# Optimization experiments

Measured on AMD Instinct MI355X. Metric: run time of the kernel, lower is better.

Reference implementation:

```python
import jax, jax.numpy as jnp
import numpy as np

B, N, C = 4, 2048, 1024
HEADS, DHEAD = 16, 64
EPS = 1e-7
SCALE = DHEAD ** (-0.5)


def setup_inputs() -> dict:
    key = jax.random.key(0)
    k1, k2, k3, k4 = jax.random.split(key, 4)
    inner = HEADS * DHEAD
    return {
        "x": jax.random.normal(k1, (B, N, C), dtype=jnp.float32),
        "gamma": jnp.ones((1, 1, C), dtype=jnp.float32),
        "Wq": jax.random.normal(k2, (inner, C), dtype=jnp.float32) * np.sqrt(1.0 / C),
        "Wkv": jax.random.normal(k3, (2 * DHEAD, C), dtype=jnp.float32) * np.sqrt(1.0 / C),
        "Wo": jax.random.normal(k4, (C, inner), dtype=jnp.float32) * np.sqrt(1.0 / inner) * 1e-5,
        "ls_scale": jnp.full((C,), 1e-4, dtype=jnp.float32),
    }


def reference(x, gamma, Wq, Wkv, Wo, ls_scale):
    # BiasFreeLayerNorm: divide by unbiased std (no mean subtraction), scale by gamma
    std = jnp.std(x, axis=-1, ddof=1, keepdims=True)
    xn = (x / (std + EPS)) * gamma
    # q from normalized x, k/v from the ORIGINAL x (kv_input = x before norm)
    q = xn @ Wq.T                       # [B, N, H*D]
    kv = x @ Wkv.T                      # [B, N, 2*D]
    k, v = kv[..., :DHEAD], kv[..., DHEAD:]  # shared single kv head (MQA)
    q = q.reshape(B, N, HEADS, DHEAD).transpose(0, 2, 1, 3) * SCALE  # [B, H, N, D]
    sim = jnp.einsum('bhid,bjd->bhij', q, k)
    attn = jax.nn.softmax(sim, axis=-1)
    out = jnp.einsum('bhij,bjd->bhid', attn, v)       # [B, H, N, D]
    out = out.transpose(0, 2, 1, 3).reshape(B, N, HEADS * DHEAD)
    out = out @ Wo.T
    return ls_scale * out
```

## Files before the change

kernel.cpp:

```cpp
#include <hip/hip_runtime.h>
#include <hip/hip_bf16.h>
#include <stdint.h>

typedef __attribute__((ext_vector_type(8))) short short8;
typedef __attribute__((ext_vector_type(4))) short short4v;
typedef __attribute__((ext_vector_type(4))) float f32x4;
typedef __attribute__((ext_vector_type(4))) unsigned short us4;

#define B_ 4
#define N_ 2048
#define C_ 1024
#define H_ 16
#define D_ 64

__device__ __forceinline__ unsigned short f2bf(float f) {
  union { float f; unsigned u; } v; v.f = f;
  unsigned u = v.u;
  u += 0x7fffu + ((u >> 16) & 1u);
  return (unsigned short)(u >> 16);
}

__device__ __forceinline__ unsigned short bfc(float f) {
  union { __hip_bfloat16 h; unsigned short u; } v;
  v.h = __float2bfloat16(f);
  return v.u;
}

__device__ __forceinline__ void glds16(const unsigned short* g, const unsigned short* l) {
  __builtin_amdgcn_global_load_lds(
      (const __attribute__((address_space(1))) void*)(uintptr_t)g,
      (__attribute__((address_space(3))) void*)(uintptr_t)l, 16, 0, 0);
}

__device__ __forceinline__ f32x4 mfma16(short8 a, short8 b, f32x4 c) {
  return __builtin_amdgcn_mfma_f32_16x16x32_bf16(a, b, c, 0, 0, 0);
}

#if __has_builtin(__builtin_amdgcn_mfma_f32_16x16x16bf16_1k)
__device__ __forceinline__ f32x4 mfma16b(short4v a, short4v b, f32x4 c) {
  return __builtin_amdgcn_mfma_f32_16x16x16bf16_1k(a, b, c, 0, 0, 0);
}
#else
__device__ __forceinline__ f32x4 mfma16b(short4v a, short4v b, f32x4 c) {
  asm volatile("v_mfma_f32_16x16x16_bf16 %0, %1, %2, %0\n\ts_nop 7\n\ts_nop 7"
               : "+v"(c) : "v"(a), "v"(b));
  return c;
}
#endif

__global__ __launch_bounds__(256) void prep_cast_k(const float* __restrict__ x,
                                                   const float* __restrict__ gamma,
                                                   unsigned short* __restrict__ xb,
                                                   float* __restrict__ rstd_v,
                                                   const float* __restrict__ wq,
                                                   const float* __restrict__ wkv,
                                                   const float* __restrict__ wo,
                                                   unsigned short* __restrict__ dq,
                                                   unsigned short* __restrict__ dkv,
                                                   unsigned short* __restrict__ dwo) {
  const int t = threadIdx.x;
  if (blockIdx.x >= 8192) {
    const int i = (blockIdx.x - 8192) * 256 + t;
    if (i < 262144) {
      const float4 v = ((const float4*)wq)[i];
      const float4 gv = ((const float4*)gamma)[i & 255];
      us4 o;
      o.x = f2bf(v.x * gv.x); o.y = f2bf(v.y * gv.y);
      o.z = f2bf(v.z * gv.z); o.w = f2bf(v.w * gv.w);
      ((us4*)dq)[i] = o;
    } else {
      const float* s;
      unsigned short* d;
      int j;
      if (i < 294912) { s = wkv; d = dkv; j = i - 262144; }
      else { s = wo; d = dwo; j = i - 294912; }
      const float4 v = ((const float4*)s)[j];
      us4 o; o.x = f2bf(v.x); o.y = f2bf(v.y); o.z = f2bf(v.z); o.w = f2bf(v.w);
      ((us4*)d)[j] = o;
    }
    return;
  }
  const int row = blockIdx.x;
  const float4 v = ((const float4*)(x + (size_t)row * C_))[t];
  float s1 = v.x + v.y + v.z + v.w;
  float s2 = v.x * v.x + v.y * v.y + v.z * v.z + v.w * v.w;
#pragma unroll
  for (int off = 32; off > 0; off >>= 1) {
    s1 += __shfl_down(s1, off);
    s2 += __shfl_down(s2, off);
  }
  __shared__ float r1[4], r2[4];
  if ((t & 63) == 0) { r1[t >> 6] = s1; r2[t >> 6] = s2; }
  __syncthreads();
  s1 = r1[0] + r1[1] + r1[2] + r1[3];
  s2 = r2[0] + r2[1] + r2[2] + r2[3];
  const float var = (s2 - s1 * s1 * (1.0f / C_)) * (1.0f / (C_ - 1));
  const float rstd = 1.0f / (sqrtf(var) + 1e-7f);
  if (t == 0) rstd_v[row] = rstd;
  us4 a;
  a.x = f2bf(v.x); a.y = f2bf(v.y); a.z = f2bf(v.z); a.w = f2bf(v.w);
  ((us4*)(xb + (size_t)row * C_))[t] = a;
}

__global__ __launch_bounds__(256, 2) void qkv_gemm(const unsigned short* __restrict__ xb,
                                                   const unsigned short* __restrict__ wq,
                                                   const unsigned short* __restrict__ wkv,
                                                   const float* __restrict__ rstd_v,
                                                   unsigned short* __restrict__ qo,
                                                   unsigned short* __restrict__ kvo,
                                                   unsigned short* __restrict__ vtb) {
  const bool iskv = (blockIdx.x == 8);
  const unsigned short* Bw = iskv ? wkv : wq;
  const int n0 = iskv ? 0 : blockIdx.x * 128;
  const int K = 1024, m0 = blockIdx.y * 128;

  __shared__ unsigned short At[128 * 32];
  __shared__ unsigned short Bt[128 * 32];
  const int t = threadIdx.x;
  const int w = t >> 6, l = t & 63;
  const int ql = l & 15, g = l >> 4;
  const int wr = (w >> 1) * 64, wc = (w & 1) * 64;

  const int pr0 = t >> 2, pb0 = t & 3;
  const int lb0 = pb0 ^ ((pr0 >> 1) & 3);
  const int pr1 = 64 + (t >> 2);
  const int lb1 = pb0 ^ ((pr1 >> 1) & 3);
  const unsigned short* Ab = xb + (size_t)m0 * K;
  const unsigned short* Bb = Bw + (size_t)n0 * K;

  f32x4 acc[4][4];
#pragma unroll
  for (int i = 0; i < 4; ++i)
#pragma unroll
    for (int j = 0; j < 4; ++j) acc[i][j] = f32x4{0.f, 0.f, 0.f, 0.f};

  for (int k0 = 0; k0 < K; k0 += 32) {
    glds16(Ab + (size_t)pr0 * K + k0 + lb0 * 8, &At[w * 512]);
    glds16(Ab + (size_t)pr1 * K + k0 + lb1 * 8, &At[2048 + w * 512]);
    glds16(Bb + (size_t)pr0 * K + k0 + lb0 * 8, &Bt[w * 512]);
    glds16(Bb + (size_t)pr1 * K + k0 + lb1 * 8, &Bt[2048 + w * 512]);
    __syncthreads();
    short8 af[4], bfr[4];
#pragma unroll
    for (int i = 0; i < 4; ++i) {
      const int row = wr + i * 16 + ql;
      af[i] = *(const short8*)&At[row * 32 + ((g ^ ((row >> 1) & 3)) * 8)];
    }
#pragma unroll
    for (int i = 0; i < 4; ++i) {
      const int row = wc + i * 16 + ql;
      bfr[i] = *(const short8*)&Bt[row * 32 + ((g ^ ((row >> 1) & 3)) * 8)];
    }
#pragma unroll
    for (int mi = 0; mi < 4; ++mi)
#pragma unroll
      for (int ni = 0; ni < 4; ++ni)
        acc[mi][ni] = mfma16(af[mi], bfr[ni], acc[mi][ni]);
    __syncthreads();
  }

  if (!iskv) {
    float rs[4][4];
#pragma unroll
    for (int mi = 0; mi < 4; ++mi)
#pragma unroll
      for (int r = 0; r < 4; ++r)
        rs[mi][r] = 0.18033688011112042f * rstd_v[m0 + wr + mi * 16 + g * 4 + r];
#pragma unroll
    for (int mi = 0; mi < 4; ++mi)
#pragma unroll
      for (int ni = 0; ni < 4; ++ni) {
        const int col = n0 + wc + ni * 16 + ql;
#pragma unroll
        for (int r = 0; r < 4; ++r) {
          const int row = m0 + wr + mi * 16 + g * 4 + r;
          qo[(size_t)row * 1024 + col] = f2bf(acc[mi][ni][r] * rs[mi][r]);
        }
      }
  } else if (wc == 0) {
#pragma unroll
    for (int mi = 0; mi < 4; ++mi)
#pragma unroll
      for (int ni = 0; ni < 4; ++ni) {
        const int col = ni * 16 + ql;
#pragma unroll
        for (int r = 0; r < 4; ++r) {
          const int row = m0 + wr + mi * 16 + g * 4 + r;
          kvo[(size_t)row * 128 + col] = f2bf(acc[mi][ni][r]);
        }
      }
  } else {
    const int brow = m0 >> 11;
    unsigned short* vb = vtb + (size_t)brow * 64 * 2048;
#pragma unroll
    for (int mi = 0; mi < 4; ++mi) {
      const int nbase = (m0 & 2047) + wr + mi * 16 + g * 4;
#pragma unroll
      for (int ni = 0; ni < 4; ++ni) {
        const int d = ni * 16 + ql;
        const int nadj = nbase ^ (((d >> 3) & 1) ? 4 : 0);
        us4 st;
        st.x = f2bf(acc[mi][ni][0]);
        st.y = f2bf(acc[mi][ni][1]);
        st.z = f2bf(acc[mi][ni][2]);
        st.w = f2bf(acc[mi][ni][3]);
        *(us4*)&vb[(size_t)d * 2048 + nadj] = st;
      }
    }
  }
}

__global__ __launch_bounds__(256, 2) void gemm_o(const unsigned short* __restrict__ A,
                                                 const unsigned short* __restrict__ Bw,
                                                 float* __restrict__ Cout,
                                                 const float* __restrict__ colscale,
                                                 int M, int N, int K) {
  __shared__ unsigned short At[128 * 32];
  __shared__ unsigned short Bt[128 * 32];
  const int t = threadIdx.x;
  const int w = t >> 6, l = t & 63;
  const int ql = l & 15, g = l >> 4;
  const int wr = (w >> 1) * 64, wc = (w & 1) * 64;
  const int m0 = blockIdx.y * 128, n0 = blockIdx.x * 128;

  const int pr0 = t >> 2, pb0 = t & 3;
  const int lb0 = pb0 ^ ((pr0 >> 1) & 3);
  const int pr1 = 64 + (t >> 2);
  const int lb1 = pb0 ^ ((pr1 >> 1) & 3);
  const unsigned short* Ab = A + (size_t)m0 * K;
  const unsigned short* Bb = Bw + (size_t)n0 * K;

  f32x4 acc[4][4];
#pragma unroll
  for (int i = 0; i < 4; ++i)
#pragma unroll
    for (int j = 0; j < 4; ++j) acc[i][j] = f32x4{0.f, 0.f, 0.f, 0.f};

  for (int k0 = 0; k0 < K; k0 += 32) {
    glds16(Ab + (size_t)pr0 * K + k0 + lb0 * 8, &At[w * 512]);
    glds16(Ab + (size_t)pr1 * K + k0 + lb1 * 8, &At[2048 + w * 512]);
    glds16(Bb + (size_t)pr0 * K + k0 + lb0 * 8, &Bt[w * 512]);
    glds16(Bb + (size_t)pr1 * K + k0 + lb1 * 8, &Bt[2048 + w * 512]);
    __syncthreads();
    short8 af[4], bfr[4];
#pragma unroll
    for (int i = 0; i < 4; ++i) {
      const int row = wr + i * 16 + ql;
      af[i] = *(const short8*)&At[row * 32 + ((g ^ ((row >> 1) & 3)) * 8)];
    }
#pragma unroll
    for (int i = 0; i < 4; ++i) {
      const int row = wc + i * 16 + ql;
      bfr[i] = *(const short8*)&Bt[row * 32 + ((g ^ ((row >> 1) & 3)) * 8)];
    }
#pragma unroll
    for (int mi = 0; mi < 4; ++mi)
#pragma unroll
      for (int ni = 0; ni < 4; ++ni)
        acc[mi][ni] = mfma16(af[mi], bfr[ni], acc[mi][ni]);
    __syncthreads();
  }

#pragma unroll
  for (int mi = 0; mi < 4; ++mi)
#pragma unroll
    for (int ni = 0; ni < 4; ++ni) {
      const int col = n0 + wc + ni * 16 + ql;
      const float cs = colscale[col];
#pragma unroll
      for (int r = 0; r < 4; ++r) {
        const int row = m0 + wr + mi * 16 + g * 4 + r;
        Cout[(size_t)row * N + col] = acc[mi][ni][r] * cs;
      }
    }
}

__global__ __launch_bounds__(256, 3) void attn_k(const unsigned short* __restrict__ qb,
                                                 const unsigned short* __restrict__ kvb,
                                                 const unsigned short* __restrict__ vtb,
                                                 unsigned short* __restrict__ ao) {
  __shared__ unsigned short Kt[2][64 * 64];
  __shared__ unsigned short Vt[2][64 * 64];

  const int idx = blockIdx.x;
  const int qc = idx & 15, hd = (idx >> 4) & 15, b = idx >> 8;
  const int t = threadIdx.x, w = t >> 6, l = t & 63;
  const int ql = l & 15, g = l >> 4;
  const int q0 = qc * 128 + w * 32;

  const unsigned short* qbase = qb + (size_t)(b * N_ + q0) * C_ + hd * D_;
  short8 Qf[2][2];
#pragma unroll
  for (int qs = 0; qs < 2; ++qs)
#pragma unroll
    for (int h = 0; h < 2; ++h)
      Qf[qs][h] = *(const short8*)(qbase + (size_t)(16 * qs + ql) * C_ + 32 * h + 8 * g);

  const unsigned short* kvrow = kvb + (size_t)(b * N_) * 128;
  const unsigned short* vtrow = vtb + (size_t)b * 64 * 2048;
  const int sr = l >> 3;
  const int blk = ((l & 7) ^ sr) << 3;
  const int row0 = 16 * w + sr;
  const int row1 = row0 + 8;
  const int sw = ql & 7;
  const int hb = (ql >> 3) & 1;

  auto stage = [&](int bi, int kt) {
    glds16(kvrow + (size_t)(kt * 64 + row0) * 128 + blk, &Kt[bi][(2 * w) * 512]);
    glds16(kvrow + (size_t)(kt * 64 + row1) * 128 + blk, &Kt[bi][(2 * w + 1) * 512]);
    glds16(vtrow + (size_t)row0 * 2048 + kt * 64 + blk, &Vt[bi][(2 * w) * 512]);
    glds16(vtrow + (size_t)row1 * 2048 + kt * 64 + blk, &Vt[bi][(2 * w + 1) * 512]);
  };

  f32x4 o[2][4];
#pragma unroll
  for (int qs = 0; qs < 2; ++qs)
#pragma unroll
    for (int dt = 0; dt < 4; ++dt) o[qs][dt] = f32x4{0.f, 0.f, 0.f, 0.f};
  float m[2] = {-1e30f, -1e30f}, lsum[2] = {0.f, 0.f};

  auto tilec = [&](int bi) {
    short8 Kf[4][2];
#pragma unroll
    for (int c = 0; c < 4; ++c) {
      const int roff = (16 * c + ql) * 64;
      Kf[c][0] = *(const short8*)&Kt[bi][roff + ((g ^ sw) << 3)];
      Kf[c][1] = *(const short8*)&Kt[bi][roff + (((g + 4) ^ sw) << 3)];
    }
    short4v pa[2][4];
#pragma unroll
    for (int qs = 0; qs < 2; ++qs) {
      f32x4 s[4];
#pragma unroll
      for (int c = 0; c < 4; ++c) {
        f32x4 acc = {0.f, 0.f, 0.f, 0.f};
        acc = mfma16(Kf[c][0], Qf[qs][0], acc);
        acc = mfma16(Kf[c][1], Qf[qs][1], acc);
        s[c] = acc;
      }
      float t0 = fmaxf(s[0][0], fmaxf(s[0][1], s[0][2]));
      float t1 = fmaxf(s[0][3], fmaxf(s[1][0], s[1][1]));
      float t2 = fmaxf(s[1][2], fmaxf(s[1][3], s[2][0]));
      float t3 = fmaxf(s[2][1], fmaxf(s[2][2], s[2][3]));
      float t4 = fmaxf(s[3][0], fmaxf(s[3][1], s[3][2]));
      float tm = fmaxf(s[3][3], fmaxf(t0, t1));
      tm = fmaxf(tm, fmaxf(t2, fmaxf(t3, t4)));
      if (!__all(tm <= m[qs] + 8.0f)) {
        float tmr = fmaxf(tm, __shfl_xor(tm, 16));
        tmr = fmaxf(tmr, __shfl_xor(tmr, 32));
        const float mn = fmaxf(m[qs], tmr);
        const float corr = __builtin_amdgcn_exp2f(m[qs] - mn);
        lsum[qs] *= corr;
#pragma unroll
        for (int dt = 0; dt < 4; ++dt) o[qs][dt] *= corr;
        m[qs] = mn;
      }
      float ps = 0.f;
#pragma unroll
      for (int c = 0; c < 4; ++c) {
        const float p0 = __builtin_amdgcn_exp2f(s[c][0] - m[qs]);
        const float p1 = __builtin_amdgcn_exp2f(s[c][1] - m[qs]);
        const float p2 = __builtin_amdgcn_exp2f(s[c][2] - m[qs]);
        const float p3 = __builtin_amdgcn_exp2f(s[c][3] - m[qs]);
        ps += (p0 + p1) + (p2 + p3);
        short4v pv;
        pv[0] = (short)bfc(p0); pv[1] = (short)bfc(p1);
        pv[2] = (short)bfc(p2); pv[3] = (short)bfc(p3);
        pa[qs][c] = pv;
      }
      lsum[qs] += ps;
    }

    __builtin_amdgcn_s_setprio(1);
#pragma unroll
    for (int dt = 0; dt < 4; ++dt) {
      const int vro = (16 * dt + ql) * 64 + 4 * ((g & 1) ^ hb);
      short4v Vf[4];
#pragma unroll
      for (int c = 0; c < 4; ++c)
        Vf[c] = *(const short4v*)&Vt[bi][vro + (((2 * c + (g >> 1)) ^ sw) << 3)];
#pragma unroll
      for (int qs = 0; qs < 2; ++qs)
#pragma unroll
        for (int c = 0; c < 4; ++c)
          o[qs][dt] = mfma16b(Vf[c], pa[qs][c], o[qs][dt]);
    }
    __builtin_amdgcn_s_setprio(0);
  };

  stage(0, 0);
  for (int kt = 0; kt < 32; kt += 2) {
    __syncthreads();
    stage(1, kt + 1);
    tilec(0);
    __syncthreads();
    if (kt + 2 < 32) stage(0, kt + 2);
    tilec(1);
  }

#pragma unroll
  for (int qs = 0; qs < 2; ++qs) {
    lsum[qs] += __shfl_xor(lsum[qs], 16);
    lsum[qs] += __shfl_xor(lsum[qs], 32);
  }

#pragma unroll
  for (int qs = 0; qs < 2; ++qs) {
    const float inv = 1.0f / lsum[qs];
    unsigned short* orow = ao + (size_t)(b * N_ + q0 + 16 * qs + ql) * C_ + hd * D_;
#pragma unroll
    for (int dt = 0; dt < 4; ++dt) {
      us4 st;
      st.x = bfc(o[qs][dt][0] * inv);
      st.y = bfc(o[qs][dt][1] * inv);
      st.z = bfc(o[qs][dt][2] * inv);
      st.w = bfc(o[qs][dt][3] * inv);
      *(us4*)(orow + dt * 16 + 4 * g) = st;
    }
  }
}

extern "C" void kernel_launch(void* const* d_in, const int* in_sizes, int n_in,
                              void* d_out, int out_size, void* d_ws, size_t ws_size,
                              hipStream_t stream) {
  const float* x = (const float*)d_in[0];
  const float* gamma = (const float*)d_in[1];
  const float* Wq = (const float*)d_in[2];
  const float* Wkv = (const float*)d_in[3];
  const float* Wo = (const float*)d_in[4];
  const float* ls = (const float*)d_in[5];
  float* out = (float*)d_out;

  unsigned short* ws = (unsigned short*)d_ws;
  const size_t R = (size_t)B_ * N_;
  unsigned short* xb = ws;
  unsigned short* qbuf = xb + R * C_;
  unsigned short* kvb = qbuf + R * C_;
  unsigned short* aob = kvb + R * 128;
  unsigned short* wqb = aob + R * C_;
  unsigned short* wkvb = wqb + (size_t)C_ * C_;
  unsigned short* wob = wkvb + (size_t)128 * C_;
  unsigned short* vtb = wob + (size_t)C_ * C_;
  float* rstd = (float*)(vtb + (size_t)4 * 64 * 2048);

  prep_cast_k<<<(int)R + 2176, 256, 0, stream>>>(x, gamma, xb, rstd,
                                                 Wq, Wkv, Wo, wqb, wkvb, wob);
  qkv_gemm<<<dim3(9, R / 128), 256, 0, stream>>>(xb, wqb, wkvb, rstd,
                                                 qbuf, kvb, vtb);
  attn_k<<<B_ * H_ * (N_ / 128), 256, 0, stream>>>(qbuf, kvb, vtb, aob);
  gemm_o<<<dim3(C_ / 128, R / 128), 256, 0, stream>>>(aob, wob, out, ls,
                                                      (int)R, C_, C_);
}
```

Measured before the change: 173.1 us.

## Split attention block across 8 waves with 16 query rows each

```diff
diff --git a/kernel.cpp b/kernel.cpp
--- a/kernel.cpp
+++ b/kernel.cpp
@@ -275,7 +275,7 @@
     }
 }
 
-__global__ __launch_bounds__(256, 3) void attn_k(const unsigned short* __restrict__ qb,
+__global__ __launch_bounds__(512, 4) void attn_k(const unsigned short* __restrict__ qb,
                                                  const unsigned short* __restrict__ kvb,
                                                  const unsigned short* __restrict__ vtb,
                                                  unsigned short* __restrict__ ao) {
@@ -286,38 +286,31 @@
   const int qc = idx & 15, hd = (idx >> 4) & 15, b = idx >> 8;
   const int t = threadIdx.x, w = t >> 6, l = t & 63;
   const int ql = l & 15, g = l >> 4;
-  const int q0 = qc * 128 + w * 32;
+  const int q0 = qc * 128 + w * 16;
 
   const unsigned short* qbase = qb + (size_t)(b * N_ + q0) * C_ + hd * D_;
-  short8 Qf[2][2];
-#pragma unroll
-  for (int qs = 0; qs < 2; ++qs)
-#pragma unroll
-    for (int h = 0; h < 2; ++h)
-      Qf[qs][h] = *(const short8*)(qbase + (size_t)(16 * qs + ql) * C_ + 32 * h + 8 * g);
+  short8 Qf[2];
+#pragma unroll
+  for (int h = 0; h < 2; ++h)
+    Qf[h] = *(const short8*)(qbase + (size_t)ql * C_ + 32 * h + 8 * g);
 
   const unsigned short* kvrow = kvb + (size_t)(b * N_) * 128;
   const unsigned short* vtrow = vtb + (size_t)b * 64 * 2048;
   const int sr = l >> 3;
   const int blk = ((l & 7) ^ sr) << 3;
-  const int row0 = 16 * w + sr;
-  const int row1 = row0 + 8;
+  const int row0 = 8 * w + sr;
   const int sw = ql & 7;
   const int hb = (ql >> 3) & 1;
 
   auto stage = [&](int bi, int kt) {
-    glds16(kvrow + (size_t)(kt * 64 + row0) * 128 + blk, &Kt[bi][(2 * w) * 512]);
-    glds16(kvrow + (size_t)(kt * 64 + row1) * 128 + blk, &Kt[bi][(2 * w + 1) * 512]);
-    glds16(vtrow + (size_t)row0 * 2048 + kt * 64 + blk, &Vt[bi][(2 * w) * 512]);
-    glds16(vtrow + (size_t)row1 * 2048 + kt * 64 + blk, &Vt[bi][(2 * w + 1) * 512]);
+    glds16(kvrow + (size_t)(kt * 64 + row0) * 128 + blk, &Kt[bi][w * 512]);
+    glds16(vtrow + (size_t)row0 * 2048 + kt * 64 + blk, &Vt[bi][w * 512]);
   };
 
-  f32x4 o[2][4];
-#pragma unroll
-  for (int qs = 0; qs < 2; ++qs)
-#pragma unroll
-    for (int dt = 0; dt < 4; ++dt) o[qs][dt] = f32x4{0.f, 0.f, 0.f, 0.f};
-  float m[2] = {-1e30f, -1e30f}, lsum[2] = {0.f, 0.f};
+  f32x4 o[4];
+#pragma unroll
+  for (int dt = 0; dt < 4; ++dt) o[dt] = f32x4{0.f, 0.f, 0.f, 0.f};
+  float m = -1e30f, lsum = 0.f;
 
   auto tilec = [&](int bi) {
     short8 Kf[4][2];
@@ -327,49 +320,46 @@
       Kf[c][0] = *(const short8*)&Kt[bi][roff + ((g ^ sw) << 3)];
       Kf[c][1] = *(const short8*)&Kt[bi][roff + (((g + 4) ^ sw) << 3)];
     }
-    short4v pa[2][4];
-#pragma unroll
-    for (int qs = 0; qs < 2; ++qs) {
-      f32x4 s[4];
-#pragma unroll
-      for (int c = 0; c < 4; ++c) {
-        f32x4 acc = {0.f, 0.f, 0.f, 0.f};
-        acc = mfma16(Kf[c][0], Qf[qs][0], acc);
-        acc = mfma16(Kf[c][1], Qf[qs][1], acc);
-        s[c] = acc;
-      }
-      float t0 = fmaxf(s[0][0], fmaxf(s[0][1], s[0][2]));
-      float t1 = fmaxf(s[0][3], fmaxf(s[1][0], s[1][1]));
-      float t2 = fmaxf(s[1][2], fmaxf(s[1][3], s[2][0]));
-      float t3 = fmaxf(s[2][1], fmaxf(s[2][2], s[2][3]));
-      float t4 = fmaxf(s[3][0], fmaxf(s[3][1], s[3][2]));
-      float tm = fmaxf(s[3][3], fmaxf(t0, t1));
-      tm = fmaxf(tm, fmaxf(t2, fmaxf(t3, t4)));
-      if (!__all(tm <= m[qs] + 8.0f)) {
-        float tmr = fmaxf(tm, __shfl_xor(tm, 16));
-        tmr = fmaxf(tmr, __shfl_xor(tmr, 32));
-        const float mn = fmaxf(m[qs], tmr);
-        const float corr = __builtin_amdgcn_exp2f(m[qs] - mn);
-        lsum[qs] *= corr;
-#pragma unroll
-        for (int dt = 0; dt < 4; ++dt) o[qs][dt] *= corr;
-        m[qs] = mn;
-      }
-      float ps = 0.f;
-#pragma unroll
-      for (int c = 0; c < 4; ++c) {
-        const float p0 = __builtin_amdgcn_exp2f(s[c][0] - m[qs]);
-        const float p1 = __builtin_amdgcn_exp2f(s[c][1] - m[qs]);
-        const float p2 = __builtin_amdgcn_exp2f(s[c][2] - m[qs]);
-        const float p3 = __builtin_amdgcn_exp2f(s[c][3] - m[qs]);
-        ps += (p0 + p1) + (p2 + p3);
-        short4v pv;
-        pv[0] = (short)bfc(p0); pv[1] = (short)bfc(p1);
-        pv[2] = (short)bfc(p2); pv[3] = (short)bfc(p3);
-        pa[qs][c] = pv;
-      }
-      lsum[qs] += ps;
-    }
+    f32x4 s[4];
+#pragma unroll
+    for (int c = 0; c < 4; ++c) {
+      f32x4 acc = {0.f, 0.f, 0.f, 0.f};
+      acc = mfma16(Kf[c][0], Qf[0], acc);
+      acc = mfma16(Kf[c][1], Qf[1], acc);
+      s[c] = acc;
+    }
+    float t0 = fmaxf(s[0][0], fmaxf(s[0][1], s[0][2]));
+    float t1 = fmaxf(s[0][3], fmaxf(s[1][0], s[1][1]));
+    float t2 = fmaxf(s[1][2], fmaxf(s[1][3], s[2][0]));
+    float t3 = fmaxf(s[2][1], fmaxf(s[2][2], s[2][3]));
+    float t4 = fmaxf(s[3][0], fmaxf(s[3][1], s[3][2]));
+    float tm = fmaxf(s[3][3], fmaxf(t0, t1));
+    tm = fmaxf(tm, fmaxf(t2, fmaxf(t3, t4)));
+    if (!__all(tm <= m + 8.0f)) {
+      float tmr = fmaxf(tm, __shfl_xor(tm, 16));
+      tmr = fmaxf(tmr, __shfl_xor(tmr, 32));
+      const float mn = fmaxf(m, tmr);
+      const float corr = __builtin_amdgcn_exp2f(m - mn);
+      lsum *= corr;
+#pragma unroll
+      for (int dt = 0; dt < 4; ++dt) o[dt] *= corr;
+      m = mn;
+    }
+    short4v pa[4];
+    float ps = 0.f;
+#pragma unroll
+    for (int c = 0; c < 4; ++c) {
+      const float p0 = __builtin_amdgcn_exp2f(s[c][0] - m);
+      const float p1 = __builtin_amdgcn_exp2f(s[c][1] - m);
+      const float p2 = __builtin_amdgcn_exp2f(s[c][2] - m);
+      const float p3 = __builtin_amdgcn_exp2f(s[c][3] - m);
+      ps += (p0 + p1) + (p2 + p3);
+      short4v pv;
+      pv[0] = (short)bfc(p0); pv[1] = (short)bfc(p1);
+      pv[2] = (short)bfc(p2); pv[3] = (short)bfc(p3);
+      pa[c] = pv;
+    }
+    lsum += ps;
 
     __builtin_amdgcn_s_setprio(1);
 #pragma unroll
@@ -380,10 +370,8 @@
       for (int c = 0; c < 4; ++c)
         Vf[c] = *(const short4v*)&Vt[bi][vro + (((2 * c + (g >> 1)) ^ sw) << 3)];
 #pragma unroll
-      for (int qs = 0; qs < 2; ++qs)
-#pragma unroll
-        for (int c = 0; c < 4; ++c)
-          o[qs][dt] = mfma16b(Vf[c], pa[qs][c], o[qs][dt]);
+      for (int c = 0; c < 4; ++c)
+        o[dt] = mfma16b(Vf[c], pa[c], o[dt]);
     }
     __builtin_amdgcn_s_setprio(0);
   };
@@ -398,25 +386,19 @@
     tilec(1);
   }
 
-#pragma unroll
-  for (int qs = 0; qs < 2; ++qs) {
-    lsum[qs] += __shfl_xor(lsum[qs], 16);
-    lsum[qs] += __shfl_xor(lsum[qs], 32);
-  }
-
-#pragma unroll
-  for (int qs = 0; qs < 2; ++qs) {
-    const float inv = 1.0f / lsum[qs];
-    unsigned short* orow = ao + (size_t)(b * N_ + q0 + 16 * qs + ql) * C_ + hd * D_;
-#pragma unroll
-    for (int dt = 0; dt < 4; ++dt) {
-      us4 st;
-      st.x = bfc(o[qs][dt][0] * inv);
-      st.y = bfc(o[qs][dt][1] * inv);
-      st.z = bfc(o[qs][dt][2] * inv);
-      st.w = bfc(o[qs][dt][3] * inv);
-      *(us4*)(orow + dt * 16 + 4 * g) = st;
-    }
+  lsum += __shfl_xor(lsum, 16);
+  lsum += __shfl_xor(lsum, 32);
+
+  const float inv = 1.0f / lsum;
+  unsigned short* orow = ao + (size_t)(b * N_ + q0 + ql) * C_ + hd * D_;
+#pragma unroll
+  for (int dt = 0; dt < 4; ++dt) {
+    us4 st;
+    st.x = bfc(o[dt][0] * inv);
+    st.y = bfc(o[dt][1] * inv);
+    st.z = bfc(o[dt][2] * inv);
+    st.w = bfc(o[dt][3] * inv);
+    *(us4*)(orow + dt * 16 + 4 * g) = st;
   }
 }
 
@@ -447,7 +429,7 @@
                                                  Wq, Wkv, Wo, wqb, wkvb, wob);
   qkv_gemm<<<dim3(9, R / 128), 256, 0, stream>>>(xb, wqb, wkvb, rstd,
                                                  qbuf, kvb, vtb);
-  attn_k<<<B_ * H_ * (N_ / 128), 256, 0, stream>>>(qbuf, kvb, vtb, aob);
+  attn_k<<<B_ * H_ * (N_ / 128), 512, 0, stream>>>(qbuf, kvb, vtb, aob);
   gemm_o<<<dim3(C_ / 128, R / 128), 256, 0, stream>>>(aob, wob, out, ls,
                                                       (int)R, C_, C_);
 }
```

After: 171.7 us. About the same (-0.8%).
